# Kernel tuning notes

Measured on AMD Instinct MI355X. Metric: run time of the kernel, lower is better.

## Reference

```python
import jax, jax.numpy as jnp
import numpy as np

N_NODES = 50000
N_EDGES = 600000
N_GRAPHS = 64
IN_CH = 768
COND = 768
HID = 128


def gcn_conv(h, src, dst, n, W, b):
    """PyG GCNConv: h' = D^-1/2 (A+I) D^-1/2 (h W) + b.
    src/dst already include self-loops."""
    h = h @ W  # [N, out]
    deg = jax.ops.segment_sum(jnp.ones_like(dst, dtype=h.dtype), dst, num_segments=n)
    dinv = jnp.where(deg > 0, jax.lax.rsqrt(jnp.where(deg > 0, deg, 1.0)), 0.0)
    norm = dinv[src] * dinv[dst]  # [E]
    msg = h[src] * norm[:, None]  # gather along edges
    out = jax.ops.segment_sum(msg, dst, num_segments=n)  # scatter-add
    return out + b


def setup_inputs() -> dict:
    key = jax.random.key(0)
    k1, k2, k3, k4, k5, k6, k7 = jax.random.split(key, 7)
    x = jax.random.normal(k1, (N_NODES, IN_CH), dtype=jnp.float32)
    edge_index = jax.random.randint(k2, (2, N_EDGES), 0, N_NODES, dtype=jnp.int64)
    substring_embed = jax.random.normal(k3, (N_GRAPHS, COND), dtype=jnp.float32)
    batch = jnp.sort(jax.random.randint(k4, (N_NODES,), 0, N_GRAPHS, dtype=jnp.int64))
    d_in = IN_CH + COND
    W1 = jax.random.normal(k5, (d_in, HID), dtype=jnp.float32) / np.sqrt(d_in)
    b1 = jnp.zeros((HID,), dtype=jnp.float32)
    W2 = jax.random.normal(k6, (HID, HID), dtype=jnp.float32) / np.sqrt(HID)
    b2 = jnp.zeros((HID,), dtype=jnp.float32)
    W_out = jax.random.normal(k7, (HID, 1), dtype=jnp.float32) / np.sqrt(HID)
    b_out = jnp.zeros((1,), dtype=jnp.float32)
    return {"x": x, "edge_index": edge_index, "substring_embed": substring_embed,
            "batch": batch, "W1": W1, "b1": b1, "W2": W2, "b2": b2,
            "W_out": W_out, "b_out": b_out}


def reference(x, edge_index, substring_embed, batch, W1, b1, W2, b2, W_out, b_out):
    n = x.shape[0]
    # add self-loops once (PyG GCNConv default add_self_loops=True)
    loops = jnp.arange(n, dtype=edge_index.dtype)
    src = jnp.concatenate([edge_index[0], loops])
    dst = jnp.concatenate([edge_index[1], loops])
    # condition gather + concat
    h = jnp.concatenate([x, substring_embed[batch]], axis=-1)  # [N, 1536]
    h = jax.nn.relu(gcn_conv(h, src, dst, n, W1, b1))
    h = jax.nn.relu(gcn_conv(h, src, dst, n, W2, b2))
    logits = (h @ W_out + b_out)[:, 0]  # [N]
    return logits
```

## Files before the change

kernel.cpp:

```cpp
#include <hip/hip_runtime.h>
#include <math.h>

#define NN 50000
#define NNP 50176
#define NE 600000
#define NG 64
#define INCH 768
#define HID 128

typedef __attribute__((ext_vector_type(8))) short bf16x8;
typedef __attribute__((ext_vector_type(4))) float f32x4;
typedef __attribute__((ext_vector_type(4))) unsigned int u32x4;
typedef unsigned short u16;
typedef unsigned int u32;
typedef unsigned long long u64;

__device__ __forceinline__ u16 f2bf(float v) {
    u32 u = __builtin_bit_cast(u32, v);
    u32 r = u + 0x7FFFu + ((u >> 16) & 1u);
    return (u16)(r >> 16);
}
__device__ __forceinline__ float bf2f(u16 h) {
    u32 u = ((u32)h) << 16;
    return __builtin_bit_cast(float, u);
}
__device__ __forceinline__ u32 cvtpk(float a, float b) {
    u32 r;
    asm("v_cvt_pk_bf16_f32 %0, %1, %2" : "=v"(r) : "v"(a), "v"(b));
    return r;
}
__device__ __forceinline__ void gl_lds16(const void* g, void* l) {
    __builtin_amdgcn_global_load_lds(
        (const __attribute__((address_space(1))) unsigned int*)g,
        (__attribute__((address_space(3))) unsigned int*)l, 16, 0, 0);
}

struct SplitA { bf16x8 h, l; };

template <bool RELU>
__device__ __forceinline__ SplitA splitA(float4 b0, float4 b1) {
    if (RELU) {
        b0.x = fmaxf(b0.x, 0.f); b0.y = fmaxf(b0.y, 0.f);
        b0.z = fmaxf(b0.z, 0.f); b0.w = fmaxf(b0.w, 0.f);
        b1.x = fmaxf(b1.x, 0.f); b1.y = fmaxf(b1.y, 0.f);
        b1.z = fmaxf(b1.z, 0.f); b1.w = fmaxf(b1.w, 0.f);
    }
    u32 h0 = cvtpk(b0.x, b0.y), h1 = cvtpk(b0.z, b0.w);
    u32 h2 = cvtpk(b1.x, b1.y), h3 = cvtpk(b1.z, b1.w);
    float r0 = b0.x - __builtin_bit_cast(float, h0 << 16);
    float r1 = b0.y - __builtin_bit_cast(float, h0 & 0xFFFF0000u);
    float r2 = b0.z - __builtin_bit_cast(float, h1 << 16);
    float r3 = b0.w - __builtin_bit_cast(float, h1 & 0xFFFF0000u);
    float r4 = b1.x - __builtin_bit_cast(float, h2 << 16);
    float r5 = b1.y - __builtin_bit_cast(float, h2 & 0xFFFF0000u);
    float r6 = b1.z - __builtin_bit_cast(float, h3 << 16);
    float r7 = b1.w - __builtin_bit_cast(float, h3 & 0xFFFF0000u);
    u32 e0 = cvtpk(r0, r1), e1 = cvtpk(r2, r3);
    u32 e2 = cvtpk(r4, r5), e3 = cvtpk(r6, r7);
    SplitA s;
    s.h = __builtin_bit_cast(bf16x8, (u32x4){h0, h1, h2, h3});
    s.l = __builtin_bit_cast(bf16x8, (u32x4){e0, e1, e2, e3});
    return s;
}

__device__ __forceinline__ bf16x8 relu8(bf16x8 a) {
    u32x4 u = __builtin_bit_cast(u32x4, a);
#pragma unroll
    for (int i = 0; i < 4; i++) {
        u32 x = u[i];
        u32 lo = (x & 0x8000u) ? 0u : (x & 0x0000FFFFu);
        u32 hi = (x & 0x80000000u) ? 0u : (x & 0xFFFF0000u);
        u[i] = lo | hi;
    }
    return __builtin_bit_cast(bf16x8, u);
}

__device__ __forceinline__ void wt_pack_item(const float* __restrict__ W,
                                             u16* __restrict__ P, int tid) {
    int l = tid & 63;
    int f = (tid >> 6) & 7;
    int c = tid >> 9;
    int n = f * 16 + (l & 15);
    int kb = c * 32 + ((l >> 4) & 3) * 8;
    u64 h0 = 0, h1 = 0, l0 = 0, l1 = 0;
#pragma unroll
    for (int e = 0; e < 8; e++) {
        float v = W[(size_t)(kb + e) * HID + n];
        u16 h = f2bf(v);
        u16 r = f2bf(v - bf2f(h));
        if (e < 4) { h0 |= (u64)h << (16 * e);       l0 |= (u64)r << (16 * e); }
        else       { h1 |= (u64)h << (16 * (e - 4)); l1 |= (u64)r << (16 * (e - 4)); }
    }
    size_t base = (size_t)c * 8192 + (size_t)f * 512 + l * 8;
    *(u64*)&P[base]          = h0;
    *(u64*)&P[base + 4]      = h1;
    *(u64*)&P[base + 4096]   = l0;
    *(u64*)&P[base + 4100]   = l1;
}

__global__ __launch_bounds__(512)
void prep_fused(int* __restrict__ counts,
                const float* __restrict__ SE, const float* __restrict__ W1,
                const float* __restrict__ W2, float* __restrict__ condW,
                u16* __restrict__ W1p, u16* __restrict__ W2p) {
    const int b = blockIdx.x, t = threadIdx.x;
    if (b < 98) {
        int i = b * 512 + t;
        if (i < NN) counts[i] = 0;
    } else if (b < 162) {
        __shared__ float se[INCH];
        __shared__ float part[4][HID];
        int g = b - 98;
        for (int i = t; i < INCH; i += 512) se[i] = SE[g * INCH + i];
        __syncthreads();
        int col = t & 127, ks = t >> 7;
        const float* Wb = W1 + (size_t)INCH * HID;
        float acc = 0.f;
        for (int k = ks * 192; k < ks * 192 + 192; k++)
            acc = fmaf(se[k], Wb[(size_t)k * HID + col], acc);
        part[ks][col] = acc;
        __syncthreads();
        if (t < HID)
            condW[g * HID + t] = part[0][t] + part[1][t] + part[2][t] + part[3][t];
    } else if (b < 186) {
        wt_pack_item(W1, W1p, (b - 162) * 512 + t);
    } else {
        wt_pack_item(W2, W2p, (b - 186) * 512 + t);
    }
}

__global__ void deg_count(const int* __restrict__ dst, int* counts) {
    int e = blockIdx.x * blockDim.x + threadIdx.x;
    if (e < NE) atomicAdd(&counts[dst[e]], 1);
}

__global__ void pscan1(const int* __restrict__ counts, int* __restrict__ row_start,
                       int* __restrict__ bsum, float* __restrict__ dinv) {
    __shared__ int sm[256];
    int t = threadIdx.x;
    int i = blockIdx.x * 256 + t;
    int v = (i < NN) ? counts[i] : 0;
    if (i < NN) dinv[i] = rsqrtf((float)v + 1.0f);
    sm[t] = v;
    __syncthreads();
#pragma unroll
    for (int off = 1; off < 256; off <<= 1) {
        int add = (t >= off) ? sm[t - off] : 0;
        __syncthreads();
        sm[t] += add;
        __syncthreads();
    }
    row_start[i] = sm[t] - v;
    if (t == 255) bsum[blockIdx.x] = sm[t];
}

__global__ void pscan23(int* __restrict__ row_start, const int* __restrict__ bsum,
                        int* __restrict__ cursor, int nb) {
    __shared__ int sm[256];
    int t = threadIdx.x, b = blockIdx.x;
    int v = (t < nb) ? bsum[t] : 0;
    sm[t] = v;
    __syncthreads();
#pragma unroll
    for (int off = 1; off < 256; off <<= 1) {
        int add = (t >= off) ? sm[t - off] : 0;
        __syncthreads();
        sm[t] += add;
        __syncthreads();
    }
    int blkoff = (b == 0) ? 0 : sm[b - 1];
    int i = b * 256 + t;
    int val = row_start[i] + blkoff;
    row_start[i] = val;
    if (i < NN) cursor[i] = val;
}

__global__ void csr_fill(const int* __restrict__ src, const int* __restrict__ dst,
                         int* __restrict__ cursor, int* __restrict__ csr_src) {
    int e = blockIdx.x * blockDim.x + threadIdx.x;
    if (e < NE) {
        int pos = atomicAdd(&cursor[dst[e]], 1);
        csr_src[pos] = src[e];
    }
}

template <int K, bool ABF16, bool RELU_A, bool ADD_COND>
__global__ __launch_bounds__(256, 2)
void mfma_gemm_pipe(const void* __restrict__ Av, const u16* __restrict__ P,
                    u16* __restrict__ Cbf, const float* __restrict__ condW,
                    const int* __restrict__ batch, const float* __restrict__ dinv,
                    int M) {
    constexpr int NC = K / 32;
    constexpr int AOPS = ABF16 ? 2 : 4;
    __shared__ u16 smem[24576];
    const int t = threadIdx.x;
    const int w = t >> 6;
    const int l = t & 63;
    const int l16 = l & 15;
    const int lq = l >> 4;
    const int m0 = blockIdx.x * 128;

    const int r0 = m0 + w * 32 + l16;
    const int r1 = r0 + 16;
    const int rc0 = r0 < M ? r0 : M - 1;
    const int rc1 = r1 < M ? r1 : M - 1;
    const float* Apf0 = (const float*)Av + (size_t)rc0 * K + lq * 8;
    const float* Apf1 = (const float*)Av + (size_t)rc1 * K + lq * 8;
    const u16*   Apb0 = (const u16*)Av + (size_t)rc0 * K + lq * 8;
    const u16*   Apb1 = (const u16*)Av + (size_t)rc1 * K + lq * 8;
    const char* Pb = (const char*)P + t * 16;

    f32x4 acc[2][8] = {};

    float4 a00, a01, a10, a11;
    bf16x8 ab0, ab1;
    if constexpr (ABF16) {
        ab0 = *(const bf16x8*)Apb0;
        ab1 = *(const bf16x8*)Apb1;
    } else {
        a00 = *(const float4*)Apf0;
        a01 = *(const float4*)(Apf0 + 4);
        a10 = *(const float4*)Apf1;
        a11 = *(const float4*)(Apf1 + 4);
    }
    __builtin_amdgcn_sched_barrier(0);
    {
        char* d0 = (char*)smem + t * 16;
#pragma unroll
        for (int i = 0; i < 4; i++) gl_lds16(Pb + i * 4096, d0 + i * 4096);
        char* d1 = (char*)smem + 16384 + t * 16;
#pragma unroll
        for (int i = 0; i < 4; i++) gl_lds16(Pb + 16384 + i * 4096, d1 + i * 4096);
    }
    __builtin_amdgcn_sched_barrier(0);

    int slot = 0;
    for (int c = 0; c < NC; ++c) {
        if (c == 0)
            asm volatile("s_waitcnt vmcnt(4)" ::: "memory");
        else if (c == NC - 1)
            asm volatile("s_waitcnt vmcnt(%0)" :: "i"(AOPS) : "memory");
        else
            asm volatile("s_waitcnt vmcnt(%0)" :: "i"(AOPS + 4) : "memory");
        __builtin_amdgcn_s_barrier();
        __builtin_amdgcn_sched_barrier(0);

        float4 n00 = a00, n01 = a01, n10 = a10, n11 = a11;
        bf16x8 nb0 = ab0, nb1 = ab1;
        if (c + 1 < NC) {
            if constexpr (ABF16) {
                nb0 = *(const bf16x8*)(Apb0 + (c + 1) * 32);
                nb1 = *(const bf16x8*)(Apb1 + (c + 1) * 32);
            } else {
                n00 = *(const float4*)(Apf0 + (c + 1) * 32);
                n01 = *(const float4*)(Apf0 + (c + 1) * 32 + 4);
                n10 = *(const float4*)(Apf1 + (c + 1) * 32);
                n11 = *(const float4*)(Apf1 + (c + 1) * 32 + 4);
            }
        }
        __builtin_amdgcn_sched_barrier(0);
        if (c + 2 < NC) {
            int nq = slot + 16384;
            if (nq >= 24576) nq -= 24576;
            const char* src = (const char*)P + (size_t)(c + 2) * 16384 + t * 16;
            char* d = (char*)smem + (size_t)nq * 2 + t * 16;
#pragma unroll
            for (int i = 0; i < 4; i++) gl_lds16(src + i * 4096, d + i * 4096);
        }
        __builtin_amdgcn_sched_barrier(0);

        bf16x8 bh[8], bl[8];
#pragma unroll
        for (int f = 0; f < 8; f++)
            bh[f] = *(const bf16x8*)&smem[slot + f * 512 + l * 8];
#pragma unroll
        for (int f = 0; f < 8; f++)
            bl[f] = *(const bf16x8*)&smem[slot + 4096 + f * 512 + l * 8];

        if constexpr (ABF16) {
            bf16x8 h0 = RELU_A ? relu8(ab0) : ab0;
            bf16x8 h1 = RELU_A ? relu8(ab1) : ab1;
#pragma unroll
            for (int f = 0; f < 8; f++) {
                acc[0][f] = __builtin_amdgcn_mfma_f32_16x16x32_bf16(h0, bh[f], acc[0][f], 0, 0, 0);
                acc[1][f] = __builtin_amdgcn_mfma_f32_16x16x32_bf16(h1, bh[f], acc[1][f], 0, 0, 0);
            }
#pragma unroll
            for (int f = 0; f < 8; f++) {
                acc[0][f] = __builtin_amdgcn_mfma_f32_16x16x32_bf16(h0, bl[f], acc[0][f], 0, 0, 0);
                acc[1][f] = __builtin_amdgcn_mfma_f32_16x16x32_bf16(h1, bl[f], acc[1][f], 0, 0, 0);
            }
        } else {
            SplitA s0 = splitA<RELU_A>(a00, a01);
            SplitA s1 = splitA<RELU_A>(a10, a11);
#pragma unroll
            for (int f = 0; f < 8; f++) {
                acc[0][f] = __builtin_amdgcn_mfma_f32_16x16x32_bf16(s0.h, bh[f], acc[0][f], 0, 0, 0);
                acc[1][f] = __builtin_amdgcn_mfma_f32_16x16x32_bf16(s1.h, bh[f], acc[1][f], 0, 0, 0);
            }
#pragma unroll
            for (int f = 0; f < 8; f++) {
                acc[0][f] = __builtin_amdgcn_mfma_f32_16x16x32_bf16(s0.l, bh[f], acc[0][f], 0, 0, 0);
                acc[1][f] = __builtin_amdgcn_mfma_f32_16x16x32_bf16(s1.l, bh[f], acc[1][f], 0, 0, 0);
            }
#pragma unroll
            for (int f = 0; f < 8; f++) {
                acc[0][f] = __builtin_amdgcn_mfma_f32_16x16x32_bf16(s0.h, bl[f], acc[0][f], 0, 0, 0);
                acc[1][f] = __builtin_amdgcn_mfma_f32_16x16x32_bf16(s1.h, bl[f], acc[1][f], 0, 0, 0);
            }
        }

        a00 = n00; a01 = n01; a10 = n10; a11 = n11;
        ab0 = nb0; ab1 = nb1;
        slot += 8192;
        if (slot >= 24576) slot = 0;
    }
    __syncthreads();

    u16* lds = smem + w * 4224;
#pragma unroll
    for (int s = 0; s < 2; s++) {
#pragma unroll
        for (int j = 0; j < 4; j++) {
            int rl = s * 16 + lq * 4 + j;
            int grow = m0 + w * 32 + rl;
            int gs = grow < M ? grow : M - 1;
            float scale = dinv[gs];
            int gb = 0;
            if (ADD_COND) gb = batch[gs];
#pragma unroll
            for (int f = 0; f < 8; f++) {
                float v = acc[s][f][j];
                if (ADD_COND) v += condW[gb * HID + f * 16 + l16];
                lds[rl * 132 + f * 16 + l16] = f2bf(v * scale);
            }
        }
    }
#pragma unroll
    for (int pass = 0; pass < 8; pass++) {
        int row = pass * 4 + lq;
        bf16x8 v = *(const bf16x8*)&lds[row * 132 + l16 * 8];
        *(bf16x8*)&Cbf[(size_t)(m0 + w * 32 + row) * HID + l16 * 8] = v;
    }
}

template <int MODE>
__global__ __launch_bounds__(512)
void agg_gather(const u32* __restrict__ u, const float* __restrict__ dinv,
                const int* __restrict__ row_start, const int* __restrict__ csr_src,
                const float* __restrict__ bias, u32* __restrict__ outbf,
                const float* __restrict__ Wout, const float* __restrict__ bout,
                float* __restrict__ logits) {
    int node = blockIdx.x * 8 + (threadIdx.x >> 6);
    int lane = threadIdx.x & 63;
    if (node >= NN) return;
    int p = row_start[node], pend = row_start[node + 1];
    u32 pv = u[(size_t)node * 64 + lane];
    float ax = __builtin_bit_cast(float, pv << 16);
    float ay = __builtin_bit_cast(float, pv & 0xFFFF0000u);
    int p8 = p + ((pend - p) & ~7);
    for (; p < p8; p += 8) {
        int s0 = csr_src[p],     s1 = csr_src[p + 1];
        int s2 = csr_src[p + 2], s3 = csr_src[p + 3];
        int s4 = csr_src[p + 4], s5 = csr_src[p + 5];
        int s6 = csr_src[p + 6], s7 = csr_src[p + 7];
        u32 v0 = u[(size_t)s0 * 64 + lane];
        u32 v1 = u[(size_t)s1 * 64 + lane];
        u32 v2 = u[(size_t)s2 * 64 + lane];
        u32 v3 = u[(size_t)s3 * 64 + lane];
        u32 v4 = u[(size_t)s4 * 64 + lane];
        u32 v5 = u[(size_t)s5 * 64 + lane];
        u32 v6 = u[(size_t)s6 * 64 + lane];
        u32 v7 = u[(size_t)s7 * 64 + lane];
        ax += __builtin_bit_cast(float, v0 << 16);
        ay += __builtin_bit_cast(float, v0 & 0xFFFF0000u);
        ax += __builtin_bit_cast(float, v1 << 16);
        ay += __builtin_bit_cast(float, v1 & 0xFFFF0000u);
        ax += __builtin_bit_cast(float, v2 << 16);
        ay += __builtin_bit_cast(float, v2 & 0xFFFF0000u);
        ax += __builtin_bit_cast(float, v3 << 16);
        ay += __builtin_bit_cast(float, v3 & 0xFFFF0000u);
        ax += __builtin_bit_cast(float, v4 << 16);
        ay += __builtin_bit_cast(float, v4 & 0xFFFF0000u);
        ax += __builtin_bit_cast(float, v5 << 16);
        ay += __builtin_bit_cast(float, v5 & 0xFFFF0000u);
        ax += __builtin_bit_cast(float, v6 << 16);
        ay += __builtin_bit_cast(float, v6 & 0xFFFF0000u);
        ax += __builtin_bit_cast(float, v7 << 16);
        ay += __builtin_bit_cast(float, v7 & 0xFFFF0000u);
    }
    int p4 = p + ((pend - p) & ~3);
    for (; p < p4; p += 4) {
        int s0 = csr_src[p],     s1 = csr_src[p + 1];
        int s2 = csr_src[p + 2], s3 = csr_src[p + 3];
        u32 v0 = u[(size_t)s0 * 64 + lane];
        u32 v1 = u[(size_t)s1 * 64 + lane];
        u32 v2 = u[(size_t)s2 * 64 + lane];
        u32 v3 = u[(size_t)s3 * 64 + lane];
        ax += __builtin_bit_cast(float, v0 << 16);
        ay += __builtin_bit_cast(float, v0 & 0xFFFF0000u);
        ax += __builtin_bit_cast(float, v1 << 16);
        ay += __builtin_bit_cast(float, v1 & 0xFFFF0000u);
        ax += __builtin_bit_cast(float, v2 << 16);
        ay += __builtin_bit_cast(float, v2 & 0xFFFF0000u);
        ax += __builtin_bit_cast(float, v3 << 16);
        ay += __builtin_bit_cast(float, v3 & 0xFFFF0000u);
    }
    for (; p < pend; ++p) {
        int s = csr_src[p];
        u32 v = u[(size_t)s * 64 + lane];
        ax += __builtin_bit_cast(float, v << 16);
        ay += __builtin_bit_cast(float, v & 0xFFFF0000u);
    }
    float dd = dinv[node];
    float2 bb = *(const float2*)&bias[lane * 2];
    float ox = fmaf(dd, ax, bb.x);
    float oy = fmaf(dd, ay, bb.y);
    if (MODE == 1) {
        float2 wv = *(const float2*)&Wout[lane * 2];
        float v = fmaxf(ox, 0.f) * wv.x + fmaxf(oy, 0.f) * wv.y;
#pragma unroll
        for (int o = 32; o; o >>= 1) v += __shfl_down(v, o);
        if (lane == 0) logits[node] = v + bout[0];
    } else {
        outbf[(size_t)node * 64 + lane] = cvtpk(ox, oy);
    }
}

extern "C" void kernel_launch(void* const* d_in, const int* in_sizes, int n_in,
                              void* d_out, int out_size, void* d_ws, size_t ws_size,
                              hipStream_t stream) {
    const float* x     = (const float*)d_in[0];
    const int*   ei    = (const int*)d_in[1];
    const float* se    = (const float*)d_in[2];
    const int*   batch = (const int*)d_in[3];
    const float* W1    = (const float*)d_in[4];
    const float* b1    = (const float*)d_in[5];
    const float* W2    = (const float*)d_in[6];
    const float* b2    = (const float*)d_in[7];
    const float* Wout  = (const float*)d_in[8];
    const float* bout  = (const float*)d_in[9];
    float* logits = (float*)d_out;

    const int* srcp = ei;
    const int* dstp = ei + NE;

    float* ws       = (float*)d_ws;
    float* dinv     = ws;
    float* condW    = ws + 50176;
    u16*   W1p      = (u16*)(ws + 58368);
    u16*   W2p      = (u16*)(ws + 156672);
    int*   counts   = (int*)(ws + 173056);
    int*   row_st   = (int*)(ws + 223232);
    int*   csr_src  = (int*)(ws + 273408);
    int*   bsum     = (int*)(ws + 873408);
    float* bufA     = ws + 873664;

    u16* ubf  = (u16*)bufA;
    u16* h1bf = (u16*)(bufA + (size_t)NNP * 64);

    const int NB = (NN + 255) / 256;

    prep_fused<<<190, 512, 0, stream>>>(counts, se, W1, W2, condW, W1p, W2p);

    deg_count<<<(NE + 255) / 256, 256, 0, stream>>>(dstp, counts);
    pscan1<<<NB, 256, 0, stream>>>(counts, row_st, bsum, dinv);
    pscan23<<<NB, 256, 0, stream>>>(row_st, bsum, counts, NB);
    csr_fill<<<(NE + 255) / 256, 256, 0, stream>>>(srcp, dstp, counts, csr_src);

    const int GB = (NN + 127) / 128;

    mfma_gemm_pipe<INCH, false, false, true><<<GB, 256, 0, stream>>>(
        x, W1p, ubf, condW, batch, dinv, NN);
    agg_gather<0><<<(NN + 7) / 8, 512, 0, stream>>>(
        (const u32*)ubf, dinv, row_st, csr_src, b1, (u32*)h1bf,
        nullptr, nullptr, nullptr);

    mfma_gemm_pipe<HID, true, true, false><<<GB, 256, 0, stream>>>(
        h1bf, W2p, ubf, nullptr, nullptr, dinv, NN);
    agg_gather<1><<<(NN + 7) / 8, 512, 0, stream>>>(
        (const u32*)ubf, dinv, row_st, csr_src, b2, nullptr, Wout, bout, logits);
}
```

Measured before the change: 193.3 us.

## Merge CSR construction kernels into one cooperative kernel with grid syncs

Replaces the separate degree-count, two prefix-scan and CSR-fill kernels, plus the counts zeroing done in the prep kernel, with a single cooperative kernel that uses grid-wide syncs between phases. This removes several kernel launches and the gaps between them. In exchange, only 196 blocks of 256 threads handle the 600k edges with grid-stride loops, so each phase has less parallelism, and the grid syncs add their own cost.

Result: slower. 282.8 us (+46.3%).

```diff
diff --git a/kernel.cpp b/kernel.cpp
--- a/kernel.cpp
+++ b/kernel.cpp
@@ -1,5 +1,8 @@
 #include <hip/hip_runtime.h>
+#include <hip/hip_cooperative_groups.h>
 #include <math.h>
+
+namespace cg = cooperative_groups;
 
 #define NN 50000
 #define NNP 50176
@@ -99,18 +102,14 @@
 }
 
 __global__ __launch_bounds__(512)
-void prep_fused(int* __restrict__ counts,
-                const float* __restrict__ SE, const float* __restrict__ W1,
+void prep_fused(const float* __restrict__ SE, const float* __restrict__ W1,
                 const float* __restrict__ W2, float* __restrict__ condW,
                 u16* __restrict__ W1p, u16* __restrict__ W2p) {
     const int b = blockIdx.x, t = threadIdx.x;
-    if (b < 98) {
-        int i = b * 512 + t;
-        if (i < NN) counts[i] = 0;
-    } else if (b < 162) {
+    if (b < 64) {
         __shared__ float se[INCH];
         __shared__ float part[4][HID];
-        int g = b - 98;
+        int g = b;
         for (int i = t; i < INCH; i += 512) se[i] = SE[g * INCH + i];
         __syncthreads();
         int col = t & 127, ks = t >> 7;
@@ -122,25 +121,32 @@
         __syncthreads();
         if (t < HID)
             condW[g * HID + t] = part[0][t] + part[1][t] + part[2][t] + part[3][t];
-    } else if (b < 186) {
-        wt_pack_item(W1, W1p, (b - 162) * 512 + t);
+    } else if (b < 88) {
+        wt_pack_item(W1, W1p, (b - 64) * 512 + t);
     } else {
-        wt_pack_item(W2, W2p, (b - 186) * 512 + t);
-    }
-}
-
-__global__ void deg_count(const int* __restrict__ dst, int* counts) {
-    int e = blockIdx.x * blockDim.x + threadIdx.x;
-    if (e < NE) atomicAdd(&counts[dst[e]], 1);
-}
-
-__global__ void pscan1(const int* __restrict__ counts, int* __restrict__ row_start,
-                       int* __restrict__ bsum, float* __restrict__ dinv) {
+        wt_pack_item(W2, W2p, (b - 88) * 512 + t);
+    }
+}
+
+__global__ __launch_bounds__(256)
+void csr_build(const int* __restrict__ src, const int* __restrict__ dst,
+               int* __restrict__ counts, int* __restrict__ row_start,
+               int* __restrict__ bsum, float* __restrict__ dinv,
+               int* __restrict__ csr_src) {
+    cg::grid_group grid = cg::this_grid();
     __shared__ int sm[256];
-    int t = threadIdx.x;
-    int i = blockIdx.x * 256 + t;
-    int v = (i < NN) ? counts[i] : 0;
-    if (i < NN) dinv[i] = rsqrtf((float)v + 1.0f);
+    const int t = threadIdx.x, b = blockIdx.x;
+    const int gid = b * 256 + t;
+    const int gsz = 196 * 256;
+
+    if (gid < NN) counts[gid] = 0;
+    grid.sync();
+
+    for (int e = gid; e < NE; e += gsz) atomicAdd(&counts[dst[e]], 1);
+    grid.sync();
+
+    int v = (gid < NN) ? counts[gid] : 0;
+    if (gid < NN) dinv[gid] = rsqrtf((float)v + 1.0f);
     sm[t] = v;
     __syncthreads();
 #pragma unroll
@@ -150,16 +156,13 @@
         sm[t] += add;
         __syncthreads();
     }
-    row_start[i] = sm[t] - v;
-    if (t == 255) bsum[blockIdx.x] = sm[t];
-}
-
-__global__ void pscan23(int* __restrict__ row_start, const int* __restrict__ bsum,
-                        int* __restrict__ cursor, int nb) {
-    __shared__ int sm[256];
-    int t = threadIdx.x, b = blockIdx.x;
-    int v = (t < nb) ? bsum[t] : 0;
-    sm[t] = v;
+    int local_excl = sm[t] - v;
+    if (t == 255) bsum[b] = sm[t];
+    grid.sync();
+
+    int w = (t < 196) ? bsum[t] : 0;
+    __syncthreads();
+    sm[t] = w;
     __syncthreads();
 #pragma unroll
     for (int off = 1; off < 256; off <<= 1) {
@@ -169,17 +172,13 @@
         __syncthreads();
     }
     int blkoff = (b == 0) ? 0 : sm[b - 1];
-    int i = b * 256 + t;
-    int val = row_start[i] + blkoff;
-    row_start[i] = val;
-    if (i < NN) cursor[i] = val;
-}
-
-__global__ void csr_fill(const int* __restrict__ src, const int* __restrict__ dst,
-                         int* __restrict__ cursor, int* __restrict__ csr_src) {
-    int e = blockIdx.x * blockDim.x + threadIdx.x;
-    if (e < NE) {
-        int pos = atomicAdd(&cursor[dst[e]], 1);
+    int val = local_excl + blkoff;
+    row_start[gid] = val;
+    if (gid < NN) counts[gid] = val;
+    grid.sync();
+
+    for (int e = gid; e < NE; e += gsz) {
+        int pos = atomicAdd(&counts[dst[e]], 1);
         csr_src[pos] = src[e];
     }
 }
@@ -459,14 +458,15 @@
     u16* ubf  = (u16*)bufA;
     u16* h1bf = (u16*)(bufA + (size_t)NNP * 64);
 
-    const int NB = (NN + 255) / 256;
-
-    prep_fused<<<190, 512, 0, stream>>>(counts, se, W1, W2, condW, W1p, W2p);
-
-    deg_count<<<(NE + 255) / 256, 256, 0, stream>>>(dstp, counts);
-    pscan1<<<NB, 256, 0, stream>>>(counts, row_st, bsum, dinv);
-    pscan23<<<NB, 256, 0, stream>>>(row_st, bsum, counts, NB);
-    csr_fill<<<(NE + 255) / 256, 256, 0, stream>>>(srcp, dstp, counts, csr_src);
+    prep_fused<<<92, 512, 0, stream>>>(se, W1, W2, condW, W1p, W2p);
+
+    {
+        void* args[] = {(void*)&srcp, (void*)&dstp, (void*)&counts,
+                        (void*)&row_st, (void*)&bsum, (void*)&dinv,
+                        (void*)&csr_src};
+        hipLaunchCooperativeKernel((void*)csr_build, dim3(196), dim3(256),
+                                   args, 0, stream);
+    }
 
     const int GB = (NN + 127) / 128;
 
```
